# Kernel tuning notes

Measured on AMD Instinct MI355X. Metric: run time of the kernel, lower is better.

Reference implementation:

```python
import jax, jax.numpy as jnp
import numpy as np

N_ATOMS = 50000
N_EDGES = 1600000
DIM = 128
N_FILTERS = 128
OUT_DIM = 128
N_GAUSS = 50
CUTOFF = 10.0
LOG2 = float(np.log(2.0))


def ssp(x):
    # ShiftedSoftplus: softplus(x) - log(2)
    return jax.nn.softplus(x) - LOG2


def setup_inputs() -> dict:
    key = jax.random.key(0)
    ks = jax.random.split(key, 10)
    inp = {}
    inp["x"] = jax.random.normal(ks[0], (N_ATOMS, DIM), dtype=jnp.float32)
    inp["r_ij"] = jax.random.uniform(ks[1], (N_EDGES,), dtype=jnp.float32) * CUTOFF
    inp["f_ij"] = jax.random.normal(ks[2], (N_EDGES, N_GAUSS), dtype=jnp.float32)
    inp["ind_i"] = jax.random.randint(ks[3], (N_EDGES,), 0, N_ATOMS)
    inp["ind_j"] = jax.random.randint(ks[4], (N_EDGES,), 0, N_ATOMS)
    # filter network: Linear(50,128) + SSP + Linear(128,128) + SSP
    inp["Wf1"] = jax.random.normal(ks[5], (N_GAUSS, N_FILTERS), dtype=jnp.float32) / np.sqrt(N_GAUSS)
    inp["bf1"] = jnp.zeros((N_FILTERS,), dtype=jnp.float32)
    inp["Wf2"] = jax.random.normal(ks[6], (N_FILTERS, N_FILTERS), dtype=jnp.float32) / np.sqrt(N_FILTERS)
    inp["bf2"] = jnp.zeros((N_FILTERS,), dtype=jnp.float32)
    # in2f: Linear(dim, n_filters, bias=False)
    inp["Win"] = jax.random.normal(ks[7], (DIM, N_FILTERS), dtype=jnp.float32) / np.sqrt(DIM)
    # f2out: Linear(n_filters, out_dim) + SSP
    inp["Wout"] = jax.random.normal(ks[8], (N_FILTERS, OUT_DIM), dtype=jnp.float32) / np.sqrt(N_FILTERS)
    inp["bout"] = jnp.zeros((OUT_DIM,), dtype=jnp.float32)
    return inp


def reference(x, r_ij, f_ij, ind_i, ind_j, Wf1, bf1, Wf2, bf2, Win, Wout, bout):
    # filter network on edge features: [E, n_gauss] -> [E, n_filters]
    W = ssp(f_ij @ Wf1 + bf1)
    W = ssp(W @ Wf2 + bf2)
    # cosine cutoff: [E]
    C = 0.5 * (jnp.cos(r_ij * (jnp.pi / CUTOFF)) + 1.0)
    C = C * (r_ij < CUTOFF).astype(C.dtype)
    W = W * C[:, None]
    # node projection: [N, dim] -> [N, n_filters]
    h = x @ Win
    # gather neighbor features, apply filter, scatter-add by ind_i
    m = h[ind_j] * W                                   # [E, n_filters]
    agg = jax.ops.segment_sum(m, ind_i, num_segments=x.shape[0])  # [N, n_filters]
    # f2out: Linear + ShiftedSoftplus
    return ssp(agg @ Wout + bout)
```

## Files before the change

### kernel.cpp

```cpp
#include <hip/hip_runtime.h>
#include <math.h>

#define N_ATOMS 50000
#define N_EDGES 1600000
#define NF 128
#define NG 50
#define ITERS 4
#define EPB 512
#define LOG2F_ 0.69314718055994530942f
#define PI_OVER_CUT 0.31415926535897932f
#define CUTOFF_F 10.0f

typedef _Float16 half_t;
typedef _Float16 f16x8 __attribute__((ext_vector_type(8)));
typedef _Float16 f16x2 __attribute__((ext_vector_type(2)));
typedef float f32x4 __attribute__((ext_vector_type(4)));
typedef unsigned int u32x4 __attribute__((ext_vector_type(4)));

__device__ __forceinline__ float sspf_fast(float x) {
    float e = __expf(-fabsf(x));
    float l = __logf(1.0f + e);
    return fmaxf(x, 0.0f) + (l - LOG2F_);
}

__device__ __forceinline__ unsigned short f2h_bits(float x) {
    half_t h = (half_t)x;
    return __builtin_bit_cast(unsigned short, h);
}

__device__ __forceinline__ unsigned int pk2(float a, float b) {
    return __builtin_bit_cast(unsigned int, __builtin_amdgcn_cvt_pkrtz(a, b));
}

template <bool BIAS_SSP, bool IN_HALF, bool OUT_HALF>
__global__ __launch_bounds__(256) void gemm128_kernel(
    const void* __restrict__ Xv, const float* __restrict__ W,
    const float* __restrict__ bias, void* __restrict__ Yv, int N) {
    __shared__ float xs[32][128];
    const int row0 = blockIdx.x * 32;
    const int tid = threadIdx.x;

    if (IN_HALF) {
        const half_t* X = (const half_t*)Xv;
        for (int i = tid; i < 32 * 16; i += 256) {
            int r = i >> 4;
            f16x8 v = {0, 0, 0, 0, 0, 0, 0, 0};
            if (row0 + r < N) v = *((const f16x8*)(X + (size_t)row0 * 128) + i);
            #pragma unroll
            for (int e = 0; e < 8; ++e) xs[r][(i & 15) * 8 + e] = (float)v[e];
        }
    } else {
        const float4* src = (const float4*)((const float*)Xv + (size_t)row0 * 128);
        float4* dst = (float4*)(&xs[0][0]);
        for (int i = tid; i < 32 * 32; i += 256) {
            int r = i >> 5;
            float4 v = {0.f, 0.f, 0.f, 0.f};
            if (row0 + r < N) v = src[i];
            dst[i] = v;
        }
    }
    __syncthreads();

    const int rq = tid >> 5;
    const int cq = tid & 31;
    float4 a0 = {0,0,0,0}, a1 = {0,0,0,0}, a2 = {0,0,0,0}, a3 = {0,0,0,0};
    const float4* Wv = (const float4*)W;

    #pragma unroll 4
    for (int k = 0; k < 128; ++k) {
        float4 w = Wv[k * 32 + cq];
        float x0 = xs[rq * 4 + 0][k];
        float x1 = xs[rq * 4 + 1][k];
        float x2 = xs[rq * 4 + 2][k];
        float x3 = xs[rq * 4 + 3][k];
        a0.x += x0 * w.x; a0.y += x0 * w.y; a0.z += x0 * w.z; a0.w += x0 * w.w;
        a1.x += x1 * w.x; a1.y += x1 * w.y; a1.z += x1 * w.z; a1.w += x1 * w.w;
        a2.x += x2 * w.x; a2.y += x2 * w.y; a2.z += x2 * w.z; a2.w += x2 * w.w;
        a3.x += x3 * w.x; a3.y += x3 * w.y; a3.z += x3 * w.z; a3.w += x3 * w.w;
    }

    float4 bq = {0,0,0,0};
    if (BIAS_SSP) bq = ((const float4*)bias)[cq];
    #pragma unroll
    for (int i = 0; i < 4; ++i) {
        float4 v = (i == 0) ? a0 : (i == 1) ? a1 : (i == 2) ? a2 : a3;
        int r = row0 + rq * 4 + i;
        if (r >= N) continue;
        if (BIAS_SSP) {
            v.x = sspf_fast(v.x + bq.x); v.y = sspf_fast(v.y + bq.y);
            v.z = sspf_fast(v.z + bq.z); v.w = sspf_fast(v.w + bq.w);
        }
        if (OUT_HALF) {
            uint2 st = { pk2(v.x, v.y), pk2(v.z, v.w) };
            *(uint2*)((half_t*)Yv + (size_t)r * 128 + cq * 4) = st;
        } else {
            ((float4*)((float*)Yv + (size_t)r * 128))[cq] = v;
        }
    }
}

__global__ __launch_bounds__(256) void preconv_kernel(
    const float* __restrict__ Wf1, const float* __restrict__ Wf2,
    half_t* __restrict__ w1t, half_t* __restrict__ w2t) {
    int id = blockIdx.x * 256 + threadIdx.x;
    if (id < 128 * 64) {
        int col = id >> 6, k = id & 63;
        w1t[id] = (k < NG) ? (half_t)Wf1[k * NF + col] : (half_t)0.0f;
    } else if (id < 128 * 64 + 128 * 128) {
        int t = id - 128 * 64;
        int col = t >> 7, k = t & 127;
        w2t[t] = (half_t)Wf2[k * NF + col];
    }
}

#define OFF_W2T   16384
#define OFF_W1OUT 49152

__global__ __launch_bounds__(512, 4) void edge_kernel(
    const float* __restrict__ f_ij, const float* __restrict__ r_ij,
    const int* __restrict__ ind_i, const int* __restrict__ ind_j,
    const half_t* __restrict__ w1t_g, const half_t* __restrict__ w2t_g,
    const float* __restrict__ bf1, const float* __restrict__ bf2,
    const half_t* __restrict__ h, half_t* __restrict__ agg) {
    __shared__ __align__(16) unsigned char lds[81920];
    const int tid = threadIdx.x;

    for (int c = tid; c < 1024; c += 512) {
        int col = c >> 3, kc = c & 7;
        u32x4 v = ((const u32x4*)w1t_g)[c];
        *(u32x4*)(lds + (col << 7) + ((kc ^ (col & 7)) << 4)) = v;
    }
    for (int c = tid; c < 2048; c += 512) {
        int col = c >> 4, kc = c & 15;
        u32x4 v = ((const u32x4*)w2t_g)[c];
        int slot = (kc & 8) | ((kc & 7) ^ (col & 7));
        *(u32x4*)(lds + OFF_W2T + (col << 8) + (slot << 4)) = v;
    }

    const int lane = tid & 63;
    const int wid = tid >> 6;
    const int l15 = lane & 15;
    const int lg  = lane >> 4;
    const int l7  = lane & 7;
    const int h3  = l15 >> 3;
    const int hb  = (l7 >> 2) & 1;
    const int lgl = lg ^ (l7 & 3);
    const int par = lane & 1;

    float b1r[8], b2r[8];
    #pragma unroll
    for (int t = 0; t < 8; ++t) {
        b1r[t] = bf1[t * 16 + l15];
        b2r[t] = bf2[t * 16 + l15];
    }

    const int b1b0 = (l15 << 7) + (hb << 6) + (lgl << 4);
    const int b1b1 = (l15 << 7) + ((hb ^ 1) << 6) + (lgl << 4);
    const int b2b0 = OFF_W2T + (l15 << 8) + (hb << 6) + (lgl << 4);
    const int b2b1 = OFF_W2T + (l15 << 8) + ((hb ^ 1) << 6) + (lgl << 4);
    const int a2b0 = OFF_W1OUT + wid * 4096 + (l15 << 8) + (hb << 6) + (lgl << 4);
    const int a2b1 = OFF_W1OUT + wid * 4096 + (l15 << 8) + ((hb ^ 1) << 6) + (lgl << 4);
    const int ep1base = OFF_W1OUT + wid * 4096 + lg * 1024 + l7 * 2;
    const int rw4 = (lg & 1) * 4;

    const int bb = blockIdx.x * EPB;
    const float* aptr = f_ij + (size_t)(bb + wid * 16 + l15) * NG + lg * 8;

    __syncthreads();

    for (int it = 0; it < ITERS; ++it) {
        const int eb = bb + it * 128 + wid * 16;
        const int erow = eb + lg * 4;

        float rv[4]; int jv[4], iv[4];
        #pragma unroll
        for (int r = 0; r < 4; ++r) {
            rv[r] = r_ij[erow + r];
            jv[r] = ind_j[erow + r];
            iv[r] = ind_i[erow + r];
        }

        float2 q[8];
        #pragma unroll
        for (int p = 0; p < 4; ++p) q[p] = *(const float2*)(aptr + 2 * p);
        #pragma unroll
        for (int p = 0; p < 4; ++p) {
            float2 v = {0.f, 0.f};
            if (lg * 8 + 2 * p <= 16) v = *(const float2*)(aptr + 32 + 2 * p);
            q[4 + p] = v;
        }
        aptr += (size_t)128 * NG;

        unsigned int hd[4][4];
        #pragma unroll
        for (int r = 0; r < 4; ++r) {
            const unsigned int* hrow = (const unsigned int*)(h + (size_t)jv[r] * NF);
            #pragma unroll
            for (int u = 0; u < 4; ++u)
                hd[r][u] = hrow[(par ? (4 + u) * 8 : u * 8) + (l15 >> 1)];
        }

        f16x8 a1[2];
        #pragma unroll
        for (int ks = 0; ks < 2; ++ks) {
            #pragma unroll
            for (int p = 0; p < 4; ++p) {
                f16x2 hvv = __builtin_bit_cast(f16x2,
                    __builtin_amdgcn_cvt_pkrtz(q[ks * 4 + p].x, q[ks * 4 + p].y));
                a1[ks][2 * p]     = hvv[0];
                a1[ks][2 * p + 1] = hvv[1];
            }
        }

        f32x4 acc1[8];
        #pragma unroll
        for (int t = 0; t < 8; ++t) acc1[t] = (f32x4){0.f, 0.f, 0.f, 0.f};
        #pragma unroll
        for (int t = 0; t < 8; ++t) {
            f16x8 b0 = *(const f16x8*)(lds + b1b0 + t * 2048);
            f16x8 b1 = *(const f16x8*)(lds + b1b1 + t * 2048);
            acc1[t] = __builtin_amdgcn_mfma_f32_16x16x32_f16(a1[0], b0, acc1[t], 0, 0, 0);
            acc1[t] = __builtin_amdgcn_mfma_f32_16x16x32_f16(a1[1], b1, acc1[t], 0, 0, 0);
        }

        #pragma unroll
        for (int t = 0; t < 8; ++t) {
            #pragma unroll
            for (int r = 0; r < 4; ++r) {
                unsigned short bits = f2h_bits(sspf_fast(acc1[t][r] + b1r[t]));
                int slotx = (2 * (t & 3) + h3) ^ (rw4 + r);
                *(unsigned short*)(lds + ep1base + r * 256 + ((t >> 2) << 7) + (slotx << 4)) = bits;
            }
        }

        f32x4 acc2[8];
        #pragma unroll
        for (int t = 0; t < 8; ++t) acc2[t] = (f32x4){0.f, 0.f, 0.f, 0.f};
        f16x8 a2[4];
        #pragma unroll
        for (int ks = 0; ks < 4; ++ks) {
            int addr = ((ks & 1) ? a2b1 : a2b0) + (ks >> 1) * 128;
            a2[ks] = *(const f16x8*)(lds + addr);
        }
        #pragma unroll
        for (int t = 0; t < 8; ++t) {
            #pragma unroll
            for (int ks = 0; ks < 4; ++ks) {
                int addr = ((ks & 1) ? b2b1 : b2b0) + (ks >> 1) * 128 + t * 4096;
                f16x8 b = *(const f16x8*)(lds + addr);
                acc2[t] = __builtin_amdgcn_mfma_f32_16x16x32_f16(a2[ks], b, acc2[t], 0, 0, 0);
            }
        }

        #pragma unroll
        for (int r = 0; r < 4; ++r) {
            float c = 0.5f * (__cosf(rv[r] * PI_OVER_CUT) + 1.0f);
            c = (rv[r] < CUTOFF_F) ? c : 0.0f;
            float w2v[8];
            #pragma unroll
            for (int t = 0; t < 8; ++t) w2v[t] = sspf_fast(acc2[t][r] + b2r[t]) * c;
            half_t* arow = agg + (size_t)iv[r] * NF;
            #pragma unroll
            for (int u = 0; u < 4; ++u) {
                float send = par ? w2v[u] : w2v[4 + u];
                float recv = __shfl_xor(send, 1);
                float wA = par ? recv : w2v[u];
                float wB = par ? w2v[4 + u] : recv;
                f16x2 hp = __builtin_bit_cast(f16x2, hd[r][u]);
                unsigned int pk = pk2((float)hp[0] * wA, (float)hp[1] * wB);
                int t = par ? 4 + u : u;
                half_t* ap = arow + t * 16 + (l15 & ~1);
                asm volatile("global_atomic_pk_add_f16 %0, %1, off"
                             :: "v"(ap), "v"(pk) : "memory");
            }
        }
    }
}

extern "C" void kernel_launch(void* const* d_in, const int* in_sizes, int n_in,
                              void* d_out, int out_size, void* d_ws, size_t ws_size,
                              hipStream_t stream) {
    const float* x     = (const float*)d_in[0];
    const float* r_ij  = (const float*)d_in[1];
    const float* f_ij  = (const float*)d_in[2];
    const int*   ind_i = (const int*)d_in[3];
    const int*   ind_j = (const int*)d_in[4];
    const float* Wf1   = (const float*)d_in[5];
    const float* bf1   = (const float*)d_in[6];
    const float* Wf2   = (const float*)d_in[7];
    const float* bf2   = (const float*)d_in[8];
    const float* Win   = (const float*)d_in[9];
    const float* Wout  = (const float*)d_in[10];
    const float* bout  = (const float*)d_in[11];
    float* out = (float*)d_out;

    half_t* agg = (half_t*)d_ws;
    half_t* h   = agg + (size_t)N_ATOMS * NF;
    half_t* w1t = h + (size_t)N_ATOMS * NF;
    half_t* w2t = w1t + 128 * 64;

    (void)hipMemsetAsync(agg, 0, (size_t)N_ATOMS * NF * sizeof(half_t), stream);

    preconv_kernel<<<96, 256, 0, stream>>>(Wf1, Wf2, w1t, w2t);

    const int gemm_blocks = (N_ATOMS + 31) / 32;
    gemm128_kernel<false, false, true><<<gemm_blocks, 256, 0, stream>>>(
        x, Win, nullptr, h, N_ATOMS);

    edge_kernel<<<N_EDGES / EPB, 512, 0, stream>>>(f_ij, r_ij, ind_i, ind_j,
                                                   w1t, w2t, bf1, bf2, h, agg);

    gemm128_kernel<true, true, false><<<gemm_blocks, 256, 0, stream>>>(
        agg, Wout, bout, out, N_ATOMS);
}
```

Baseline: 773.8 us.

## Read filter weights from global memory instead of LDS, shrink edge blocks

The edge kernel no longer stages the transposed Wf1/Wf2 half weights in LDS. Each wave now reads its MFMA B operands directly from global memory, relying on L1/L2 caching. That drops the LDS staging loop and the block barrier, and LDS use shrinks to 16 KB for the per-wave intermediate tile. Blocks are reduced to 256 threads handling 256 edges, with launch bounds raised to 5 blocks per CU for higher occupancy. In exchange, every MFMA step now issues vector-memory loads for weights that used to be cheap LDS reads.

Result: slower. 1.700 ms (+119.7%).

```diff
diff --git a/kernel.cpp b/kernel.cpp
--- a/kernel.cpp
+++ b/kernel.cpp
@@ -6,7 +6,7 @@
 #define NF 128
 #define NG 50
 #define ITERS 4
-#define EPB 512
+#define EPB 256
 #define LOG2F_ 0.69314718055994530942f
 #define PI_OVER_CUT 0.31415926535897932f
 #define CUTOFF_F 10.0f
@@ -15,7 +15,6 @@
 typedef _Float16 f16x8 __attribute__((ext_vector_type(8)));
 typedef _Float16 f16x2 __attribute__((ext_vector_type(2)));
 typedef float f32x4 __attribute__((ext_vector_type(4)));
-typedef unsigned int u32x4 __attribute__((ext_vector_type(4)));
 
 __device__ __forceinline__ float sspf_fast(float x) {
     float e = __expf(-fabsf(x));
@@ -113,29 +112,14 @@
     }
 }
 
-#define OFF_W2T   16384
-#define OFF_W1OUT 49152
-
-__global__ __launch_bounds__(512, 4) void edge_kernel(
+__global__ __launch_bounds__(256, 5) void edge_kernel(
     const float* __restrict__ f_ij, const float* __restrict__ r_ij,
     const int* __restrict__ ind_i, const int* __restrict__ ind_j,
     const half_t* __restrict__ w1t_g, const half_t* __restrict__ w2t_g,
     const float* __restrict__ bf1, const float* __restrict__ bf2,
     const half_t* __restrict__ h, half_t* __restrict__ agg) {
-    __shared__ __align__(16) unsigned char lds[81920];
+    __shared__ __align__(16) unsigned char lds[16384];
     const int tid = threadIdx.x;
-
-    for (int c = tid; c < 1024; c += 512) {
-        int col = c >> 3, kc = c & 7;
-        u32x4 v = ((const u32x4*)w1t_g)[c];
-        *(u32x4*)(lds + (col << 7) + ((kc ^ (col & 7)) << 4)) = v;
-    }
-    for (int c = tid; c < 2048; c += 512) {
-        int col = c >> 4, kc = c & 15;
-        u32x4 v = ((const u32x4*)w2t_g)[c];
-        int slot = (kc & 8) | ((kc & 7) ^ (col & 7));
-        *(u32x4*)(lds + OFF_W2T + (col << 8) + (slot << 4)) = v;
-    }
 
     const int lane = tid & 63;
     const int wid = tid >> 6;
@@ -154,22 +138,19 @@
         b2r[t] = bf2[t * 16 + l15];
     }
 
-    const int b1b0 = (l15 << 7) + (hb << 6) + (lgl << 4);
-    const int b1b1 = (l15 << 7) + ((hb ^ 1) << 6) + (lgl << 4);
-    const int b2b0 = OFF_W2T + (l15 << 8) + (hb << 6) + (lgl << 4);
-    const int b2b1 = OFF_W2T + (l15 << 8) + ((hb ^ 1) << 6) + (lgl << 4);
-    const int a2b0 = OFF_W1OUT + wid * 4096 + (l15 << 8) + (hb << 6) + (lgl << 4);
-    const int a2b1 = OFF_W1OUT + wid * 4096 + (l15 << 8) + ((hb ^ 1) << 6) + (lgl << 4);
-    const int ep1base = OFF_W1OUT + wid * 4096 + lg * 1024 + l7 * 2;
+    const half_t* w1p = w1t_g + l15 * 64 + lg * 8;
+    const half_t* w2p = w2t_g + l15 * 128 + lg * 8;
+
+    const int a2b0 = wid * 4096 + (l15 << 8) + (hb << 6) + (lgl << 4);
+    const int a2b1 = wid * 4096 + (l15 << 8) + ((hb ^ 1) << 6) + (lgl << 4);
+    const int ep1base = wid * 4096 + lg * 1024 + l7 * 2;
     const int rw4 = (lg & 1) * 4;
 
     const int bb = blockIdx.x * EPB;
     const float* aptr = f_ij + (size_t)(bb + wid * 16 + l15) * NG + lg * 8;
 
-    __syncthreads();
-
     for (int it = 0; it < ITERS; ++it) {
-        const int eb = bb + it * 128 + wid * 16;
+        const int eb = bb + it * 64 + wid * 16;
         const int erow = eb + lg * 4;
 
         float rv[4]; int jv[4], iv[4];
@@ -189,7 +170,7 @@
             if (lg * 8 + 2 * p <= 16) v = *(const float2*)(aptr + 32 + 2 * p);
             q[4 + p] = v;
         }
-        aptr += (size_t)128 * NG;
+        aptr += (size_t)64 * NG;
 
         unsigned int hd[4][4];
         #pragma unroll
@@ -217,8 +198,8 @@
         for (int t = 0; t < 8; ++t) acc1[t] = (f32x4){0.f, 0.f, 0.f, 0.f};
         #pragma unroll
         for (int t = 0; t < 8; ++t) {
-            f16x8 b0 = *(const f16x8*)(lds + b1b0 + t * 2048);
-            f16x8 b1 = *(const f16x8*)(lds + b1b1 + t * 2048);
+            f16x8 b0 = *(const f16x8*)(w1p + t * 1024);
+            f16x8 b1 = *(const f16x8*)(w1p + t * 1024 + 32);
             acc1[t] = __builtin_amdgcn_mfma_f32_16x16x32_f16(a1[0], b0, acc1[t], 0, 0, 0);
             acc1[t] = __builtin_amdgcn_mfma_f32_16x16x32_f16(a1[1], b1, acc1[t], 0, 0, 0);
         }
@@ -246,8 +227,7 @@
         for (int t = 0; t < 8; ++t) {
             #pragma unroll
             for (int ks = 0; ks < 4; ++ks) {
-                int addr = ((ks & 1) ? b2b1 : b2b0) + (ks >> 1) * 128 + t * 4096;
-                f16x8 b = *(const f16x8*)(lds + addr);
+                f16x8 b = *(const f16x8*)(w2p + t * 2048 + ks * 32);
                 acc2[t] = __builtin_amdgcn_mfma_f32_16x16x32_f16(a2[ks], b, acc2[t], 0, 0, 0);
             }
         }
@@ -307,7 +287,7 @@
     gemm128_kernel<false, false, true><<<gemm_blocks, 256, 0, stream>>>(
         x, Win, nullptr, h, N_ATOMS);
 
-    edge_kernel<<<N_EDGES / EPB, 512, 0, stream>>>(f_ij, r_ij, ind_i, ind_j,
+    edge_kernel<<<N_EDGES / EPB, 256, 0, stream>>>(f_ij, r_ij, ind_i, ind_j,
                                                    w1t, w2t, bf1, bf2, h, agg);
 
     gemm128_kernel<true, true, false><<<gemm_blocks, 256, 0, stream>>>(
```

## Keep filter activations in registers via transposed MFMA and fold bias1 into weights

Applied to the files above, without the earlier changes.

The edge kernel swaps MFMA operand roles so the first layer's output lands edge-per-column. Lane shuffles then rebuild the second layer's B operand in registers, which removes the LDS round trip and the per-wave staging buffer. Bias1 is folded into the first weight matrix as an extra K row paired with a constant-1 input, and LDS shrinks so occupancy can rise to 6 blocks. Aggregation switches from packed fp16 atomics to fp32 atomicAdd, which doubles the number of atomic ops and the agg memory traffic but improves accumulation precision.

Measured after the change: 2.890 ms. 3.73x slower.

```diff
diff --git a/kernel.cpp b/kernel.cpp
--- a/kernel.cpp
+++ b/kernel.cpp
@@ -15,6 +15,7 @@
 typedef _Float16 f16x8 __attribute__((ext_vector_type(8)));
 typedef _Float16 f16x2 __attribute__((ext_vector_type(2)));
 typedef float f32x4 __attribute__((ext_vector_type(4)));
+typedef unsigned int u32;
 typedef unsigned int u32x4 __attribute__((ext_vector_type(4)));
 
 __device__ __forceinline__ float sspf_fast(float x) {
@@ -23,13 +24,8 @@
     return fmaxf(x, 0.0f) + (l - LOG2F_);
 }
 
-__device__ __forceinline__ unsigned short f2h_bits(float x) {
-    half_t h = (half_t)x;
-    return __builtin_bit_cast(unsigned short, h);
-}
-
-__device__ __forceinline__ unsigned int pk2(float a, float b) {
-    return __builtin_bit_cast(unsigned int, __builtin_amdgcn_cvt_pkrtz(a, b));
+__device__ __forceinline__ u32 pk2(float a, float b) {
+    return __builtin_bit_cast(u32, __builtin_amdgcn_cvt_pkrtz(a, b));
 }
 
 template <bool BIAS_SSP, bool IN_HALF, bool OUT_HALF>
@@ -100,12 +96,16 @@
 }
 
 __global__ __launch_bounds__(256) void preconv_kernel(
-    const float* __restrict__ Wf1, const float* __restrict__ Wf2,
+    const float* __restrict__ Wf1, const float* __restrict__ bf1,
+    const float* __restrict__ Wf2,
     half_t* __restrict__ w1t, half_t* __restrict__ w2t) {
     int id = blockIdx.x * 256 + threadIdx.x;
     if (id < 128 * 64) {
         int col = id >> 6, k = id & 63;
-        w1t[id] = (k < NG) ? (half_t)Wf1[k * NF + col] : (half_t)0.0f;
+        float v = 0.0f;
+        if (k < NG) v = Wf1[k * NF + col];
+        else if (k == NG) v = bf1[col];
+        w1t[id] = (half_t)v;
     } else if (id < 128 * 64 + 128 * 128) {
         int t = id - 128 * 64;
         int col = t >> 7, k = t & 127;
@@ -113,16 +113,15 @@
     }
 }
 
-#define OFF_W2T   16384
-#define OFF_W1OUT 49152
-
-__global__ __launch_bounds__(512, 4) void edge_kernel(
+#define OFF_W2T 16384
+
+__global__ __launch_bounds__(512, 6) void edge_kernel(
     const float* __restrict__ f_ij, const float* __restrict__ r_ij,
     const int* __restrict__ ind_i, const int* __restrict__ ind_j,
     const half_t* __restrict__ w1t_g, const half_t* __restrict__ w2t_g,
-    const float* __restrict__ bf1, const float* __restrict__ bf2,
-    const half_t* __restrict__ h, half_t* __restrict__ agg) {
-    __shared__ __align__(16) unsigned char lds[81920];
+    const float* __restrict__ bf2,
+    const half_t* __restrict__ h, float* __restrict__ agg) {
+    __shared__ __align__(16) unsigned char lds[49152];
     const int tid = threadIdx.x;
 
     for (int c = tid; c < 1024; c += 512) {
@@ -142,26 +141,23 @@
     const int l15 = lane & 15;
     const int lg  = lane >> 4;
     const int l7  = lane & 7;
-    const int h3  = l15 >> 3;
     const int hb  = (l7 >> 2) & 1;
     const int lgl = lg ^ (l7 & 3);
-    const int par = lane & 1;
-
-    float b1r[8], b2r[8];
+    const int ghi = lg >> 1;
+    const int god = lg & 1;
+
+    u32 b2h[16];
     #pragma unroll
     for (int t = 0; t < 8; ++t) {
-        b1r[t] = bf1[t * 16 + l15];
-        b2r[t] = bf2[t * 16 + l15];
+        const float* bp = bf2 + t * 16 + 4 * lg;
+        b2h[2 * t]     = pk2(bp[0], bp[1]);
+        b2h[2 * t + 1] = pk2(bp[2], bp[3]);
     }
 
     const int b1b0 = (l15 << 7) + (hb << 6) + (lgl << 4);
     const int b1b1 = (l15 << 7) + ((hb ^ 1) << 6) + (lgl << 4);
     const int b2b0 = OFF_W2T + (l15 << 8) + (hb << 6) + (lgl << 4);
     const int b2b1 = OFF_W2T + (l15 << 8) + ((hb ^ 1) << 6) + (lgl << 4);
-    const int a2b0 = OFF_W1OUT + wid * 4096 + (l15 << 8) + (hb << 6) + (lgl << 4);
-    const int a2b1 = OFF_W1OUT + wid * 4096 + (l15 << 8) + ((hb ^ 1) << 6) + (lgl << 4);
-    const int ep1base = OFF_W1OUT + wid * 4096 + lg * 1024 + l7 * 2;
-    const int rw4 = (lg & 1) * 4;
 
     const int bb = blockIdx.x * EPB;
     const float* aptr = f_ij + (size_t)(bb + wid * 16 + l15) * NG + lg * 8;
@@ -170,15 +166,10 @@
 
     for (int it = 0; it < ITERS; ++it) {
         const int eb = bb + it * 128 + wid * 16;
-        const int erow = eb + lg * 4;
-
-        float rv[4]; int jv[4], iv[4];
-        #pragma unroll
-        for (int r = 0; r < 4; ++r) {
-            rv[r] = r_ij[erow + r];
-            jv[r] = ind_j[erow + r];
-            iv[r] = ind_i[erow + r];
-        }
+
+        float rvv = r_ij[eb + l15];
+        int jvv = ind_j[eb + l15];
+        int ivv = ind_i[eb + l15];
 
         float2 q[8];
         #pragma unroll
@@ -187,28 +178,20 @@
         for (int p = 0; p < 4; ++p) {
             float2 v = {0.f, 0.f};
             if (lg * 8 + 2 * p <= 16) v = *(const float2*)(aptr + 32 + 2 * p);
+            if (p == 1 && lg == 2) v.x = 1.0f;
             q[4 + p] = v;
         }
         aptr += (size_t)128 * NG;
 
-        unsigned int hd[4][4];
-        #pragma unroll
-        for (int r = 0; r < 4; ++r) {
-            const unsigned int* hrow = (const unsigned int*)(h + (size_t)jv[r] * NF);
-            #pragma unroll
-            for (int u = 0; u < 4; ++u)
-                hd[r][u] = hrow[(par ? (4 + u) * 8 : u * 8) + (l15 >> 1)];
-        }
-
-        f16x8 a1[2];
+        f16x8 fb[2];
         #pragma unroll
         for (int ks = 0; ks < 2; ++ks) {
             #pragma unroll
             for (int p = 0; p < 4; ++p) {
-                f16x2 hvv = __builtin_bit_cast(f16x2,
+                f16x2 hv = __builtin_bit_cast(f16x2,
                     __builtin_amdgcn_cvt_pkrtz(q[ks * 4 + p].x, q[ks * 4 + p].y));
-                a1[ks][2 * p]     = hvv[0];
-                a1[ks][2 * p + 1] = hvv[1];
+                fb[ks][2 * p]     = hv[0];
+                fb[ks][2 * p + 1] = hv[1];
             }
         }
 
@@ -217,62 +200,75 @@
         for (int t = 0; t < 8; ++t) acc1[t] = (f32x4){0.f, 0.f, 0.f, 0.f};
         #pragma unroll
         for (int t = 0; t < 8; ++t) {
-            f16x8 b0 = *(const f16x8*)(lds + b1b0 + t * 2048);
-            f16x8 b1 = *(const f16x8*)(lds + b1b1 + t * 2048);
-            acc1[t] = __builtin_amdgcn_mfma_f32_16x16x32_f16(a1[0], b0, acc1[t], 0, 0, 0);
-            acc1[t] = __builtin_amdgcn_mfma_f32_16x16x32_f16(a1[1], b1, acc1[t], 0, 0, 0);
-        }
-
+            f16x8 wa0 = *(const f16x8*)(lds + b1b0 + t * 2048);
+            f16x8 wa1 = *(const f16x8*)(lds + b1b1 + t * 2048);
+            acc1[t] = __builtin_amdgcn_mfma_f32_16x16x32_f16(wa0, fb[0], acc1[t], 0, 0, 0);
+            acc1[t] = __builtin_amdgcn_mfma_f32_16x16x32_f16(wa1, fb[1], acc1[t], 0, 0, 0);
+        }
+
+        u32 w[8][2];
         #pragma unroll
         for (int t = 0; t < 8; ++t) {
+            w[t][0] = pk2(sspf_fast(acc1[t][0]), sspf_fast(acc1[t][1]));
+            w[t][1] = pk2(sspf_fast(acc1[t][2]), sspf_fast(acc1[t][3]));
+        }
+
+        uint2 hq[8];
+        {
+            const uint2* hrow = (const uint2*)(h + (size_t)jvv * NF) + lg;
             #pragma unroll
-            for (int r = 0; r < 4; ++r) {
-                unsigned short bits = f2h_bits(sspf_fast(acc1[t][r] + b1r[t]));
-                int slotx = (2 * (t & 3) + h3) ^ (rw4 + r);
-                *(unsigned short*)(lds + ep1base + r * 256 + ((t >> 2) << 7) + (slotx << 4)) = bits;
-            }
-        }
-
-        f32x4 acc2[8];
-        #pragma unroll
-        for (int t = 0; t < 8; ++t) acc2[t] = (f32x4){0.f, 0.f, 0.f, 0.f};
-        f16x8 a2[4];
+            for (int t = 0; t < 8; ++t) hq[t] = hrow[4 * t];
+        }
+
+        f16x8 bbf[4];
         #pragma unroll
         for (int ks = 0; ks < 4; ++ks) {
-            int addr = ((ks & 1) ? a2b1 : a2b0) + (ks >> 1) * 128;
-            a2[ks] = *(const f16x8*)(lds + addr);
-        }
+            u32 we0 = w[2 * ks][0], we1 = w[2 * ks][1];
+            u32 wo0 = w[2 * ks + 1][0], wo1 = w[2 * ks + 1][1];
+            u32 p16a = ghi ? wo0 : we0, p16b = ghi ? wo1 : we1;
+            u32 p32a = ghi ? we0 : wo0, p32b = ghi ? we1 : wo1;
+            u32 p48a = god ? wo0 : we0, p48b = god ? wo1 : we1;
+            u32 r16a = (u32)__shfl_xor((int)p16a, 16);
+            u32 r16b = (u32)__shfl_xor((int)p16b, 16);
+            u32 r32a = (u32)__shfl_xor((int)p32a, 32);
+            u32 r32b = (u32)__shfl_xor((int)p32b, 32);
+            u32 r48a = (u32)__shfl_xor((int)p48a, 48);
+            u32 r48b = (u32)__shfl_xor((int)p48b, 48);
+            u32 sA0 = (lg == 0) ? we0 : (lg == 1) ? r48a : (lg == 2) ? r32a : r16a;
+            u32 sA1 = (lg == 0) ? we1 : (lg == 1) ? r48b : (lg == 2) ? r32b : r16b;
+            u32 sB0 = (lg == 0) ? r16a : (lg == 1) ? r32a : (lg == 2) ? r48a : wo0;
+            u32 sB1 = (lg == 0) ? r16b : (lg == 1) ? r32b : (lg == 2) ? r48b : wo1;
+            bbf[ks] = __builtin_bit_cast(f16x8, (u32x4){sA0, sA1, sB0, sB1});
+        }
+
+        float c = 0.5f * (__cosf(rvv * PI_OVER_CUT) + 1.0f);
+        c = (rvv < CUTOFF_F) ? c : 0.0f;
+
+        float* grow = agg + (size_t)ivv * NF + 4 * lg;
         #pragma unroll
         for (int t = 0; t < 8; ++t) {
-            #pragma unroll
-            for (int ks = 0; ks < 4; ++ks) {
-                int addr = ((ks & 1) ? b2b1 : b2b0) + (ks >> 1) * 128 + t * 4096;
-                f16x8 b = *(const f16x8*)(lds + addr);
-                acc2[t] = __builtin_amdgcn_mfma_f32_16x16x32_f16(a2[ks], b, acc2[t], 0, 0, 0);
-            }
-        }
-
-        #pragma unroll
-        for (int r = 0; r < 4; ++r) {
-            float c = 0.5f * (__cosf(rv[r] * PI_OVER_CUT) + 1.0f);
-            c = (rv[r] < CUTOFF_F) ? c : 0.0f;
-            float w2v[8];
-            #pragma unroll
-            for (int t = 0; t < 8; ++t) w2v[t] = sspf_fast(acc2[t][r] + b2r[t]) * c;
-            half_t* arow = agg + (size_t)iv[r] * NF;
-            #pragma unroll
-            for (int u = 0; u < 4; ++u) {
-                float send = par ? w2v[u] : w2v[4 + u];
-                float recv = __shfl_xor(send, 1);
-                float wA = par ? recv : w2v[u];
-                float wB = par ? w2v[4 + u] : recv;
-                f16x2 hp = __builtin_bit_cast(f16x2, hd[r][u]);
-                unsigned int pk = pk2((float)hp[0] * wA, (float)hp[1] * wB);
-                int t = par ? 4 + u : u;
-                half_t* ap = arow + t * 16 + (l15 & ~1);
-                asm volatile("global_atomic_pk_add_f16 %0, %1, off"
-                             :: "v"(ap), "v"(pk) : "memory");
-            }
+            f16x8 wa0 = *(const f16x8*)(lds + b2b0 + t * 4096);
+            f16x8 wa1 = *(const f16x8*)(lds + b2b1 + t * 4096);
+            f16x8 wa2 = *(const f16x8*)(lds + b2b0 + 128 + t * 4096);
+            f16x8 wa3 = *(const f16x8*)(lds + b2b1 + 128 + t * 4096);
+            f32x4 a2 = {0.f, 0.f, 0.f, 0.f};
+            a2 = __builtin_amdgcn_mfma_f32_16x16x32_f16(wa0, bbf[0], a2, 0, 0, 0);
+            a2 = __builtin_amdgcn_mfma_f32_16x16x32_f16(wa1, bbf[1], a2, 0, 0, 0);
+            a2 = __builtin_amdgcn_mfma_f32_16x16x32_f16(wa2, bbf[2], a2, 0, 0, 0);
+            a2 = __builtin_amdgcn_mfma_f32_16x16x32_f16(wa3, bbf[3], a2, 0, 0, 0);
+
+            f16x2 b2lo = __builtin_bit_cast(f16x2, b2h[2 * t]);
+            f16x2 b2hi = __builtin_bit_cast(f16x2, b2h[2 * t + 1]);
+            f16x2 hlo  = __builtin_bit_cast(f16x2, hq[t].x);
+            f16x2 hhi  = __builtin_bit_cast(f16x2, hq[t].y);
+            float m0 = sspf_fast(a2[0] + (float)b2lo[0]) * c * (float)hlo[0];
+            float m1 = sspf_fast(a2[1] + (float)b2lo[1]) * c * (float)hlo[1];
+            float m2 = sspf_fast(a2[2] + (float)b2hi[0]) * c * (float)hhi[0];
+            float m3 = sspf_fast(a2[3] + (float)b2hi[1]) * c * (float)hhi[1];
+            atomicAdd(grow + t * 16 + 0, m0);
+            atomicAdd(grow + t * 16 + 1, m1);
+            atomicAdd(grow + t * 16 + 2, m2);
+            atomicAdd(grow + t * 16 + 3, m3);
         }
     }
 }
@@ -294,22 +290,22 @@
     const float* bout  = (const float*)d_in[11];
     float* out = (float*)d_out;
 
-    half_t* agg = (half_t*)d_ws;
-    half_t* h   = agg + (size_t)N_ATOMS * NF;
+    float*  agg = (float*)d_ws;
+    half_t* h   = (half_t*)(agg + (size_t)N_ATOMS * NF);
     half_t* w1t = h + (size_t)N_ATOMS * NF;
     half_t* w2t = w1t + 128 * 64;
 
-    (void)hipMemsetAsync(agg, 0, (size_t)N_ATOMS * NF * sizeof(half_t), stream);
-
-    preconv_kernel<<<96, 256, 0, stream>>>(Wf1, Wf2, w1t, w2t);
+    (void)hipMemsetAsync(agg, 0, (size_t)N_ATOMS * NF * sizeof(float), stream);
+
+    preconv_kernel<<<96, 256, 0, stream>>>(Wf1, bf1, Wf2, w1t, w2t);
 
     const int gemm_blocks = (N_ATOMS + 31) / 32;
     gemm128_kernel<false, false, true><<<gemm_blocks, 256, 0, stream>>>(
         x, Win, nullptr, h, N_ATOMS);
 
     edge_kernel<<<N_EDGES / EPB, 512, 0, stream>>>(f_ij, r_ij, ind_i, ind_j,
-                                                   w1t, w2t, bf1, bf2, h, agg);
-
-    gemm128_kernel<true, true, false><<<gemm_blocks, 256, 0, stream>>>(
+                                                   w1t, w2t, bf2, h, agg);
+
+    gemm128_kernel<true, false, false><<<gemm_blocks, 256, 0, stream>>>(
         agg, Wout, bout, out, N_ATOMS);
 }
```

## Accumulate edge messages with fp32 atomics and raise MFMA wave priority

Applied to the files above, without the earlier changes.

Switches the scatter-add buffer from fp16 packed atomics to fp32 atomicAdd, one scalar per element, which removes the lane-pair shuffle and packing. The final GEMM now reads fp32 input. The h gather is changed to per-lane 16-bit loads. s_setprio is raised around the two MFMA loops so matrix work gets scheduling priority. In exchange the kernel issues twice as many atomics, and the memset and final read move twice the bytes for the aggregate buffer, while accuracy improves.

New measurement: 758.3 us. -2.0%, faster.

```diff
diff --git a/kernel.cpp b/kernel.cpp
--- a/kernel.cpp
+++ b/kernel.cpp
@@ -121,7 +121,7 @@
     const int* __restrict__ ind_i, const int* __restrict__ ind_j,
     const half_t* __restrict__ w1t_g, const half_t* __restrict__ w2t_g,
     const float* __restrict__ bf1, const float* __restrict__ bf2,
-    const half_t* __restrict__ h, half_t* __restrict__ agg) {
+    const half_t* __restrict__ h, float* __restrict__ agg) {
     __shared__ __align__(16) unsigned char lds[81920];
     const int tid = threadIdx.x;
 
@@ -145,7 +145,6 @@
     const int h3  = l15 >> 3;
     const int hb  = (l7 >> 2) & 1;
     const int lgl = lg ^ (l7 & 3);
-    const int par = lane & 1;
 
     float b1r[8], b2r[8];
     #pragma unroll
@@ -191,13 +190,13 @@
         }
         aptr += (size_t)128 * NG;
 
-        unsigned int hd[4][4];
+        unsigned short hs[4][8];
         #pragma unroll
         for (int r = 0; r < 4; ++r) {
-            const unsigned int* hrow = (const unsigned int*)(h + (size_t)jv[r] * NF);
-            #pragma unroll
-            for (int u = 0; u < 4; ++u)
-                hd[r][u] = hrow[(par ? (4 + u) * 8 : u * 8) + (l15 >> 1)];
+            const unsigned short* hrow =
+                (const unsigned short*)(h + (size_t)jv[r] * NF) + l15;
+            #pragma unroll
+            for (int t = 0; t < 8; ++t) hs[r][t] = hrow[t * 16];
         }
 
         f16x8 a1[2];
@@ -215,6 +214,7 @@
         f32x4 acc1[8];
         #pragma unroll
         for (int t = 0; t < 8; ++t) acc1[t] = (f32x4){0.f, 0.f, 0.f, 0.f};
+        __builtin_amdgcn_s_setprio(1);
         #pragma unroll
         for (int t = 0; t < 8; ++t) {
             f16x8 b0 = *(const f16x8*)(lds + b1b0 + t * 2048);
@@ -222,6 +222,7 @@
             acc1[t] = __builtin_amdgcn_mfma_f32_16x16x32_f16(a1[0], b0, acc1[t], 0, 0, 0);
             acc1[t] = __builtin_amdgcn_mfma_f32_16x16x32_f16(a1[1], b1, acc1[t], 0, 0, 0);
         }
+        __builtin_amdgcn_s_setprio(0);
 
         #pragma unroll
         for (int t = 0; t < 8; ++t) {
@@ -242,6 +243,7 @@
             int addr = ((ks & 1) ? a2b1 : a2b0) + (ks >> 1) * 128;
             a2[ks] = *(const f16x8*)(lds + addr);
         }
+        __builtin_amdgcn_s_setprio(1);
         #pragma unroll
         for (int t = 0; t < 8; ++t) {
             #pragma unroll
@@ -251,27 +253,18 @@
                 acc2[t] = __builtin_amdgcn_mfma_f32_16x16x32_f16(a2[ks], b, acc2[t], 0, 0, 0);
             }
         }
+        __builtin_amdgcn_s_setprio(0);
 
         #pragma unroll
         for (int r = 0; r < 4; ++r) {
             float c = 0.5f * (__cosf(rv[r] * PI_OVER_CUT) + 1.0f);
             c = (rv[r] < CUTOFF_F) ? c : 0.0f;
-            float w2v[8];
-            #pragma unroll
-            for (int t = 0; t < 8; ++t) w2v[t] = sspf_fast(acc2[t][r] + b2r[t]) * c;
-            half_t* arow = agg + (size_t)iv[r] * NF;
-            #pragma unroll
-            for (int u = 0; u < 4; ++u) {
-                float send = par ? w2v[u] : w2v[4 + u];
-                float recv = __shfl_xor(send, 1);
-                float wA = par ? recv : w2v[u];
-                float wB = par ? w2v[4 + u] : recv;
-                f16x2 hp = __builtin_bit_cast(f16x2, hd[r][u]);
-                unsigned int pk = pk2((float)hp[0] * wA, (float)hp[1] * wB);
-                int t = par ? 4 + u : u;
-                half_t* ap = arow + t * 16 + (l15 & ~1);
-                asm volatile("global_atomic_pk_add_f16 %0, %1, off"
-                             :: "v"(ap), "v"(pk) : "memory");
+            float* grow = agg + (size_t)iv[r] * NF + l15;
+            #pragma unroll
+            for (int t = 0; t < 8; ++t) {
+                float w2 = sspf_fast(acc2[t][r] + b2r[t]) * c;
+                float hf = (float)__builtin_bit_cast(half_t, hs[r][t]);
+                atomicAdd(grow + t * 16, hf * w2);
             }
         }
     }
@@ -294,12 +287,12 @@
     const float* bout  = (const float*)d_in[11];
     float* out = (float*)d_out;
 
-    half_t* agg = (half_t*)d_ws;
-    half_t* h   = agg + (size_t)N_ATOMS * NF;
+    float*  agg = (float*)d_ws;
+    half_t* h   = (half_t*)(agg + (size_t)N_ATOMS * NF);
     half_t* w1t = h + (size_t)N_ATOMS * NF;
     half_t* w2t = w1t + 128 * 64;
 
-    (void)hipMemsetAsync(agg, 0, (size_t)N_ATOMS * NF * sizeof(half_t), stream);
+    (void)hipMemsetAsync(agg, 0, (size_t)N_ATOMS * NF * sizeof(float), stream);
 
     preconv_kernel<<<96, 256, 0, stream>>>(Wf1, Wf2, w1t, w2t);
 
@@ -310,6 +303,6 @@
     edge_kernel<<<N_EDGES / EPB, 512, 0, stream>>>(f_ij, r_ij, ind_i, ind_j,
                                                    w1t, w2t, bf1, bf2, h, agg);
 
-    gemm128_kernel<true, true, false><<<gemm_blocks, 256, 0, stream>>>(
+    gemm128_kernel<true, false, false><<<gemm_blocks, 256, 0, stream>>>(
         agg, Wout, bout, out, N_ATOMS);
 }
```
